# Kernel optimization log

Measured on AMD Instinct MI355X. Metric: run time of the kernel, lower is better.

Reference implementation:

```python
import jax, jax.numpy as jnp
import numpy as np

NUM_STATION = 20
NUM_HEADS = 8
INPUT_DIM = 128
KEY_DIM = 16          # = val_dim = embed_dim // num_heads
EMBED_DIM = 128
NORM = 1.0 / np.sqrt(KEY_DIM).astype(np.float32)


def setup_inputs() -> dict:
    key = jax.random.key(0)
    ks = jax.random.split(key, 10)
    B, N, D = 32, 1024, INPUT_DIM
    q = jax.random.normal(ks[0], (B, N, D), jnp.float32)
    h = jax.random.normal(ks[1], (B, N, D), jnp.float32)
    stdv_k = 1.0 / np.sqrt(KEY_DIM)      # torch init: uniform(-1/sqrt(last_dim), ...)
    stdv_e = 1.0 / np.sqrt(EMBED_DIM)
    def U(k, shape, s):
        return jax.random.uniform(k, shape, jnp.float32, -s, s)
    pshape = (NUM_HEADS, INPUT_DIM, KEY_DIM)
    return {
        "q": q,
        "h": h,
        "W_query_custom": U(ks[2], pshape, stdv_k),
        "W_query_custom_1": U(ks[3], pshape, stdv_k),
        "W_key_custom": U(ks[4], pshape, stdv_k),
        "W_val_custom": U(ks[5], pshape, stdv_k),
        "W_query_charge_1": U(ks[6], pshape, stdv_k),
        "W_key_charge": U(ks[7], pshape, stdv_k),
        "W_val_charge": U(ks[8], pshape, stdv_k),
        "W_out": U(ks[9], (NUM_HEADS, KEY_DIM, EMBED_DIM), stdv_e),
    }


def reference(q, h, W_query_custom, W_query_custom_1, W_key_custom, W_val_custom,
              W_query_charge_1, W_key_charge, W_val_charge, W_out):
    S = NUM_STATION + 1                      # depot + stations
    h_st, h_tk = h[:, :S], h[:, S:]          # [B,S,D], [B,T,D]
    q_st, q_tk = q[:, :S], q[:, S:]

    proj = lambda x, W: jnp.einsum('bnd,hdk->hbnk', x, W)

    K_c = proj(h_tk, W_key_custom)           # [H,B,T,K]
    V_c = proj(h_tk, W_val_custom)
    K_s = proj(h_st, W_key_charge)           # [H,B,S,K]
    V_s = proj(h_st, W_val_charge)

    # task -> task attention (queries via W_query_custom_1)
    Q_tt = proj(q_tk, W_query_custom_1)
    A_tt = jax.nn.softmax(NORM * jnp.einsum('hbqk,hbtk->hbqt', Q_tt, K_c), axis=-1)
    heads_t = jnp.einsum('hbqt,hbtk->hbqk', A_tt, V_c)

    # task -> station attention (queries via W_query_custom)
    Q_ts = proj(q_tk, W_query_custom)
    A_ts = jax.nn.softmax(NORM * jnp.einsum('hbqk,hbsk->hbqs', Q_ts, K_s), axis=-1)
    heads_t = heads_t + jnp.einsum('hbqs,hbsk->hbqk', A_ts, V_s)

    # station -> task attention (queries via W_query_charge_1)
    Q_st = proj(q_st, W_query_charge_1)
    A_st = jax.nn.softmax(NORM * jnp.einsum('hbqk,hbtk->hbqt', Q_st, K_c), axis=-1)
    heads_s = jnp.einsum('hbqt,hbtk->hbqk', A_st, V_c)

    heads = jnp.concatenate([heads_s, heads_t], axis=2)   # [H,B,N,K]
    out = jnp.einsum('hbnk,hke->bne', heads, W_out)        # [B,N,E]
    return out
```

## Files before the change

### kernel.cpp

```cpp
#include <hip/hip_runtime.h>

typedef __bf16 bf16x8 __attribute__((ext_vector_type(8)));
typedef float f32x4 __attribute__((ext_vector_type(4)));
typedef float f32x16 __attribute__((ext_vector_type(16)));
typedef unsigned int uint32;
typedef unsigned short u16;

#define NST 21
#define TOK 1003
#define SCL 0.3606737602222409f

union U4B { uint4 u; bf16x8 b; };

__device__ __forceinline__ uint32 pkbf(float a, float b) {
  uint32 ua = __float_as_uint(a), ub = __float_as_uint(b);
  ua += 0x7fffu + ((ua >> 16) & 1u);
  ub += 0x7fffu + ((ub >> 16) & 1u);
  return (ua >> 16) | (ub & 0xffff0000u);
}
__device__ __forceinline__ u16 bf1(float a) {
  uint32 u = __float_as_uint(a);
  u += 0x7fffu + ((u >> 16) & 1u);
  return (u16)(u >> 16);
}
__device__ __forceinline__ uint32 pkperm(float lo, float hi) {
  return __builtin_amdgcn_perm(__float_as_uint(hi), __float_as_uint(lo), 0x07060302u);
}

__global__ __launch_bounds__(256) void prep(
    const float* __restrict__ q, const float* __restrict__ hx,
    const float* __restrict__ W0, const float* __restrict__ W1,
    const float* __restrict__ W2, const float* __restrict__ W3,
    const float* __restrict__ W4, const float* __restrict__ Wqst,
    const float* __restrict__ Wks, const float* __restrict__ Wvs,
    u16* __restrict__ WtAll, u16* __restrict__ Qm,
    u16* __restrict__ Ks, u16* __restrict__ Vs) {
  int bid = blockIdx.x, tid = threadIdx.x;
  __shared__ float xq2[2][128], xh2[2][128];
  if (bid < 40) {
    int w = bid >> 3, seg = bid & 7;
    const float* W = (w == 0) ? W0 : (w == 1) ? W1 : (w == 2) ? W2
                     : (w == 3) ? W3 : W4;
    u16* dst = WtAll + w * 16384;
#pragma unroll
    for (int it = 0; it < 8; ++it) {
      int i = seg * 2048 + it * 256 + tid;
      int inner = i & 127, outer = i >> 7;
      float v;
      if (w < 4) {
        int h = outer >> 4, k = outer & 15;
        v = W[h * 2048 + inner * 16 + k];
      } else {
        v = W[inner * 128 + outer];
      }
      dst[outer * 128 + inner] = bf1(v);
    }
  } else {
    int t2 = bid - 40;
    int sub = tid >> 7, col = tid & 127;
    int hh = col >> 4, k = col & 15;
    int bs2 = t2 * 2 + sub;
    int b2 = bs2 >> 5, s = bs2 & 31;
    if (s < NST) {
      xq2[sub][col] = q[(size_t)(b2 * 1024 + s) * 128 + col];
      xh2[sub][col] = hx[(size_t)(b2 * 1024 + s) * 128 + col];
    }
    __syncthreads();
    if (s < NST) {
      const float* Wq = Wqst + hh * 2048 + k;
      const float* Wk = Wks + hh * 2048 + k;
      const float* Wv = Wvs + hh * 2048 + k;
      float dq = 0.f, dk_ = 0.f, dv = 0.f;
#pragma unroll 8
      for (int d = 0; d < 128; ++d) {
        float xq = xq2[sub][d], xh = xh2[sub][d];
        dq = fmaf(xq, Wq[d * 16], dq);
        dk_ = fmaf(xh, Wk[d * 16], dk_);
        dv = fmaf(xh, Wv[d * 16], dv);
      }
      Qm[(((size_t)hh * 32 + b2) * 1024 + s) * 16 + k] = bf1(dq * SCL);
      Ks[(((size_t)hh * 32 + b2) * 32 + s) * 16 + k] = bf1(dk_);
      Vs[(((size_t)hh * 32 + b2) * 16 + k) * 32 + s] = bf1(dv);
    } else {
      Ks[(((size_t)hh * 32 + b2) * 32 + s) * 16 + k] = 0;
      Vs[(((size_t)hh * 32 + b2) * 16 + k) * 32 + s] = 0;
    }
  }
}

__global__ __launch_bounds__(256) void proj_pair(
    const float* __restrict__ q, const float* __restrict__ hx,
    const u16* __restrict__ WtAll, u16* __restrict__ Qm,
    u16* __restrict__ Qts, u16* __restrict__ Kc, u16* __restrict__ Vc) {
  __shared__ u16 Wl[128 * 136];
  int pg = blockIdx.x >> 9, mb = blockIdx.x & 511;
  int m0 = mb * 64;
  const float* A = pg ? hx : q;
  int tid = threadIdx.x;
  int wave = tid >> 6, lane = tid & 63;
  int quad = lane >> 4, l15 = lane & 15;
  int mrow = m0 + wave * 16 + l15;

  U4B af[4];
#pragma unroll
  for (int dk = 0; dk < 4; ++dk) {
    const float* Af = A + (size_t)mrow * 128 + dk * 32 + quad * 8;
    float4 a = *(const float4*)Af;
    float4 b = *(const float4*)(Af + 4);
    af[dk].u = make_uint4(pkbf(a.x, a.y), pkbf(a.z, a.w),
                          pkbf(b.x, b.y), pkbf(b.z, b.w));
  }

  int gbase = m0 + wave * 16 + quad * 4;
  int bb = gbase >> 10, n0 = gbase & 1023;

#pragma unroll
  for (int s = 0; s < 2; ++s) {
    int mode = pg * 2 + s;
    const u16* WtG = WtAll + mode * 16384;
    if (s) __syncthreads();
#pragma unroll
    for (int r = 0; r < 8; ++r) {
      int i = r * 256 + tid;
      int e = i >> 4, j = i & 15;
      *(uint4*)&Wl[e * 136 + j * 8] = *(const uint4*)(WtG + e * 128 + j * 8);
    }
    __syncthreads();

    f32x4 c[8];
#pragma unroll
    for (int nt = 0; nt < 8; ++nt)
#pragma unroll
      for (int r = 0; r < 4; ++r) c[nt][r] = 0.f;
#pragma unroll
    for (int dk = 0; dk < 4; ++dk)
#pragma unroll
      for (int nt = 0; nt < 8; ++nt) {
        U4B bg;
        bg.u = *(const uint4*)&Wl[(nt * 16 + l15) * 136 + dk * 32 + quad * 8];
        c[nt] = __builtin_amdgcn_mfma_f32_16x16x32_bf16(af[dk].b, bg.b, c[nt], 0, 0, 0);
      }

    if (mode == 0) {
#pragma unroll
      for (int nt = 0; nt < 8; ++nt)
#pragma unroll
        for (int r = 0; r < 4; ++r) {
          int n = n0 + r;
          if (n < NST) continue;
          Qm[(((size_t)nt * 32 + bb) * 1024 + n) * 16 + l15] = bf1(c[nt][r] * SCL);
        }
    } else if (mode == 1) {
#pragma unroll
      for (int nt = 0; nt < 8; ++nt)
#pragma unroll
        for (int r = 0; r < 4; ++r)
          Qts[(((size_t)nt * 32 + bb) * 1024 + n0 + r) * 16 + l15] =
              bf1(c[nt][r] * SCL);
    } else if (mode == 2) {
#pragma unroll
      for (int nt = 0; nt < 8; ++nt)
#pragma unroll
        for (int r = 0; r < 4; ++r)
          Kc[(((size_t)nt * 32 + bb) * 1024 + n0 + r) * 16 + l15] = bf1(c[nt][r]);
    } else {
#pragma unroll
      for (int nt = 0; nt < 8; ++nt) {
        uint2 w2 = make_uint2(pkbf(c[nt][0], c[nt][1]), pkbf(c[nt][2], c[nt][3]));
        *(uint2*)(Vc + (((size_t)nt * 32 + bb) * 16 + l15) * 1024 + n0) = w2;
      }
    }
  }
}

__global__ __launch_bounds__(256) void outproj(
    const u16* __restrict__ heads, const u16* __restrict__ WtAll,
    float* __restrict__ out) {
  __shared__ u16 Wl[128 * 136];
  const u16* WtG = WtAll + 4 * 16384;
  int tid = threadIdx.x;
#pragma unroll
  for (int r = 0; r < 8; ++r) {
    int i = r * 256 + tid;
    int e = i >> 4, j = i & 15;
    *(uint4*)&Wl[e * 136 + j * 8] = *(const uint4*)(WtG + e * 128 + j * 8);
  }
  __syncthreads();
  int wave = tid >> 6, lane = tid & 63;
  int quad = lane >> 4, l15 = lane & 15;
  int m0 = blockIdx.x * 64;
  int mrow = m0 + wave * 16 + l15;

  f32x4 c[8];
#pragma unroll
  for (int nt = 0; nt < 8; ++nt)
#pragma unroll
    for (int r = 0; r < 4; ++r) c[nt][r] = 0.f;
#pragma unroll
  for (int dk = 0; dk < 4; ++dk) {
    U4B af;
    af.u = *(const uint4*)(heads + (size_t)mrow * 128 + dk * 32 + quad * 8);
#pragma unroll
    for (int nt = 0; nt < 8; ++nt) {
      U4B bg;
      bg.u = *(const uint4*)&Wl[(nt * 16 + l15) * 136 + dk * 32 + quad * 8];
      c[nt] = __builtin_amdgcn_mfma_f32_16x16x32_bf16(af.b, bg.b, c[nt], 0, 0, 0);
    }
  }
  int gbase = m0 + wave * 16 + quad * 4;
#pragma unroll
  for (int nt = 0; nt < 8; ++nt)
#pragma unroll
    for (int r = 0; r < 4; ++r)
      out[(size_t)(gbase + r) * 128 + nt * 16 + l15] = c[nt][r];
}

__global__ __launch_bounds__(256, 8) void attn_main(
    const u16* __restrict__ Qm, const u16* __restrict__ Qts,
    const u16* __restrict__ Kc, const u16* __restrict__ Vc,
    const u16* __restrict__ Ks, const u16* __restrict__ Vs,
    u16* __restrict__ heads) {
  int bx = blockIdx.x;
  int hb = bx & 255, qc = bx >> 8;
  int h = hb >> 5, b = hb & 31;
  int tid = threadIdx.x;
  int wave = tid >> 6, lane = tid & 63;
  int l5 = lane >> 5, l31 = lane & 31;
  int quad = lane >> 4, l15 = lane & 15;

  __shared__ u16 Kl[128 * 26];
  __shared__ u16 Vl[16 * 140];
  __shared__ u16 Pt[4][32 * 36];
  __shared__ u16 KsL[32 * 26];
  __shared__ u16 VsL[16 * 44];

  const u16* Qbase = Qm + ((size_t)(h * 32 + b)) * 16384;
  const u16* QtsB = Qts + ((size_t)(h * 32 + b)) * 16384;
  const u16* Kbase = Kc + ((size_t)(h * 32 + b)) * 16384;
  const u16* Vbase = Vc + ((size_t)(h * 32 + b)) * 16384;
  const u16* KsB = Ks + (size_t)(h * 32 + b) * 512;
  const u16* VsB = Vs + (size_t)(h * 32 + b) * 512;

  if (tid < 64) {
    int key = tid >> 1, half = tid & 1;
    *(uint4*)&KsL[key * 26 + half * 8] = *(const uint4*)(KsB + key * 16 + half * 8);
  } else if (tid < 128) {
    int t = tid - 64;
    int d = t >> 2, kg = t & 3;
    *(uint4*)&VsL[d * 44 + kg * 8] = *(const uint4*)(VsB + d * 32 + kg * 8);
  }

  int qw0 = qc * 128 + wave * 32;
  U4B qf;
  qf.u = *(const uint4*)(Qbase + (size_t)(qw0 + l31) * 16 + l5 * 8);

  int skey = tid >> 1, shalf = tid & 1;
  int sd = tid >> 4, skg = tid & 15;
  uint4 kpre = *(const uint4*)(Kbase + (size_t)skey * 16 + shalf * 8);
  uint4 vpre = *(const uint4*)(Vbase + (size_t)sd * 1024 + skg * 8);

  f32x16 zero16;
#pragma unroll
  for (int i = 0; i < 16; ++i) zero16[i] = 0.f;
  U4B ones;
  ones.u = make_uint4(0x3F803F80u, 0x3F803F80u, 0x3F803F80u, 0x3F803F80u);

  f32x4 o[2], la[2];
#pragma unroll
  for (int mt = 0; mt < 2; ++mt)
#pragma unroll
    for (int r = 0; r < 4; ++r) { o[mt][r] = 0.f; la[mt][r] = 0.f; }

#pragma unroll 1
  for (int kb = 0; kb < 8; ++kb) {
    __syncthreads();
    *(uint4*)&Kl[skey * 26 + shalf * 8] = kpre;
    *(uint4*)&Vl[sd * 140 + skg * 8] = vpre;
    if (kb < 7) {
      int j0n = (kb + 1) * 128;
      kpre = *(const uint4*)(Kbase + (size_t)(j0n + skey) * 16 + shalf * 8);
      vpre = *(const uint4*)(Vbase + (size_t)sd * 1024 + j0n + skg * 8);
    }
    __syncthreads();
#pragma unroll 1
    for (int kt = 0; kt < 4; ++kt) {
      int key0 = kt * 32;
      U4B af;
      af.u = *(const uint4*)&Kl[(key0 + l31) * 26 + l5 * 8];
      f32x16 c0 =
          __builtin_amdgcn_mfma_f32_32x32x16_bf16(af.b, qf.b, zero16, 0, 0, 0);
      bool masked = (kb == 0) && (kt == 0);
#pragma unroll
      for (int g = 0; g < 4; ++g) {
        float p0 = __builtin_amdgcn_exp2f(c0[4 * g + 0]);
        float p1 = __builtin_amdgcn_exp2f(c0[4 * g + 1]);
        float p2 = __builtin_amdgcn_exp2f(c0[4 * g + 2]);
        float p3 = __builtin_amdgcn_exp2f(c0[4 * g + 3]);
        if (masked) {
          int kb0 = 8 * g + 4 * l5;
          p0 = (kb0 + 0 < NST) ? 0.f : p0;
          p1 = (kb0 + 1 < NST) ? 0.f : p1;
          p2 = (kb0 + 2 < NST) ? 0.f : p2;
          p3 = (kb0 + 3 < NST) ? 0.f : p3;
        }
        uint2 w2 = make_uint2(pkperm(p0, p1), pkperm(p2, p3));
        *(uint2*)&Pt[wave][l31 * 36 + 4 * l5 + 8 * g] = w2;
      }
      U4B vf;
      vf.u = *(const uint4*)&Vl[l15 * 140 + key0 + quad * 8];
#pragma unroll
      for (int mt = 0; mt < 2; ++mt) {
        U4B pf;
        pf.u = *(const uint4*)&Pt[wave][(mt * 16 + l15) * 36 + quad * 8];
        o[mt] = __builtin_amdgcn_mfma_f32_16x16x32_bf16(pf.b, vf.b, o[mt], 0, 0, 0);
        la[mt] =
            __builtin_amdgcn_mfma_f32_16x16x32_bf16(pf.b, ones.b, la[mt], 0, 0, 0);
      }
    }
  }

  f32x4 o2[2], la2[2];
#pragma unroll
  for (int mt = 0; mt < 2; ++mt)
#pragma unroll
    for (int r = 0; r < 4; ++r) { o2[mt][r] = 0.f; la2[mt][r] = 0.f; }
  qf.u = *(const uint4*)(QtsB + (size_t)(qw0 + l31) * 16 + l5 * 8);
  {
    U4B af;
    af.u = *(const uint4*)&KsL[l31 * 26 + l5 * 8];
    f32x16 c0 =
        __builtin_amdgcn_mfma_f32_32x32x16_bf16(af.b, qf.b, zero16, 0, 0, 0);
#pragma unroll
    for (int g = 0; g < 4; ++g) {
      float p0 = __builtin_amdgcn_exp2f(c0[4 * g + 0]);
      float p1 = __builtin_amdgcn_exp2f(c0[4 * g + 1]);
      float p2 = __builtin_amdgcn_exp2f(c0[4 * g + 2]);
      float p3 = __builtin_amdgcn_exp2f(c0[4 * g + 3]);
      int kb0 = 8 * g + 4 * l5;
      p0 = (kb0 + 0 >= NST) ? 0.f : p0;
      p1 = (kb0 + 1 >= NST) ? 0.f : p1;
      p2 = (kb0 + 2 >= NST) ? 0.f : p2;
      p3 = (kb0 + 3 >= NST) ? 0.f : p3;
      uint2 w2 = make_uint2(pkperm(p0, p1), pkperm(p2, p3));
      *(uint2*)&Pt[wave][l31 * 36 + 4 * l5 + 8 * g] = w2;
    }
    U4B vf;
    vf.u = *(const uint4*)&VsL[l15 * 44 + quad * 8];
#pragma unroll
    for (int mt = 0; mt < 2; ++mt) {
      U4B pf;
      pf.u = *(const uint4*)&Pt[wave][(mt * 16 + l15) * 36 + quad * 8];
      o2[mt] = __builtin_amdgcn_mfma_f32_16x16x32_bf16(pf.b, vf.b, o2[mt], 0, 0, 0);
      la2[mt] =
          __builtin_amdgcn_mfma_f32_16x16x32_bf16(pf.b, ones.b, la2[mt], 0, 0, 0);
    }
  }

#pragma unroll
  for (int mt = 0; mt < 2; ++mt)
#pragma unroll
    for (int r = 0; r < 4; ++r) {
      int n = qw0 + mt * 16 + quad * 4 + r;
      float val = o[mt][r] * __builtin_amdgcn_rcpf(la[mt][r]);
      if (n >= NST) val += o2[mt][r] * __builtin_amdgcn_rcpf(la2[mt][r]);
      heads[((size_t)b * 1024 + n) * 128 + h * 16 + l15] = bf1(val);
    }
}

extern "C" void kernel_launch(void* const* d_in, const int* in_sizes, int n_in,
                              void* d_out, int out_size, void* d_ws,
                              size_t ws_size, hipStream_t stream) {
  (void)in_sizes; (void)n_in; (void)out_size; (void)ws_size;
  const float* q     = (const float*)d_in[0];
  const float* hx    = (const float*)d_in[1];
  const float* W_qts = (const float*)d_in[2];
  const float* W_qtt = (const float*)d_in[3];
  const float* W_kc  = (const float*)d_in[4];
  const float* W_vc  = (const float*)d_in[5];
  const float* W_qst = (const float*)d_in[6];
  const float* W_ks  = (const float*)d_in[7];
  const float* W_vs  = (const float*)d_in[8];
  const float* W_out = (const float*)d_in[9];

  char* ws = (char*)d_ws;
  u16* heads = (u16*)(ws + 0);
  u16* Qm    = (u16*)(ws + 16777216);
  u16* Qts   = (u16*)(ws + 25165824);
  u16* Kc    = (u16*)(ws + 33554432);
  u16* Vc    = (u16*)(ws + 41943040);
  u16* Ks    = (u16*)(ws + 50331648);
  u16* Vs    = (u16*)(ws + 50593792);
  u16* WtAll = (u16*)(ws + 50855936);

  hipLaunchKernelGGL(prep, dim3(552), dim3(256), 0, stream,
                     q, hx, W_qtt, W_qts, W_kc, W_vc, W_out, W_qst, W_ks, W_vs,
                     WtAll, Qm, Ks, Vs);
  hipLaunchKernelGGL(proj_pair, dim3(1024), dim3(256), 0, stream,
                     q, hx, WtAll, Qm, Qts, Kc, Vc);
  hipLaunchKernelGGL(attn_main, dim3(2048), dim3(256), 0, stream,
                     Qm, Qts, Kc, Vc, Ks, Vs, heads);
  hipLaunchKernelGGL(outproj, dim3(512), dim3(256), 0, stream,
                     heads, WtAll, (float*)d_out);
}
```

Baseline: 169.5 us.

## Keep attention probabilities in registers via permlane32 swap and 32x32 PV MFMA

Removes the per-wave shared-memory staging of the probability tile. The packed bf16 probabilities are rearranged across lanes with v_permlane32_swap and fed straight as the B operand of 32x32x16 MFMAs against V^T. A row of ones is appended to V in LDS so the softmax denominator comes out of the same MFMA, replacing the separate ones-MFMAs. The station-attention pass moves ahead of the main loop, and the output is written with packed vector stores. This cuts LDS traffic and MFMA count but relies on the permlane lane layout being correct and enlarges the V LDS tiles.

```diff
diff --git a/kernel.cpp b/kernel.cpp
--- a/kernel.cpp
+++ b/kernel.cpp
@@ -25,6 +25,15 @@
 }
 __device__ __forceinline__ uint32 pkperm(float lo, float hi) {
   return __builtin_amdgcn_perm(__float_as_uint(hi), __float_as_uint(lo), 0x07060302u);
+}
+__device__ __forceinline__ void plswap(uint32& a, uint32& b) {
+#if __has_builtin(__builtin_amdgcn_permlane32_swap)
+  typedef unsigned int uu2 __attribute__((ext_vector_type(2)));
+  uu2 r = __builtin_amdgcn_permlane32_swap(a, b, false, false);
+  a = r.x; b = r.y;
+#else
+  asm volatile("v_permlane32_swap_b32 %0, %1" : "+v"(a), "+v"(b));
+#endif
 }
 
 __global__ __launch_bounds__(256) void prep(
@@ -226,13 +235,11 @@
   int tid = threadIdx.x;
   int wave = tid >> 6, lane = tid & 63;
   int l5 = lane >> 5, l31 = lane & 31;
-  int quad = lane >> 4, l15 = lane & 15;
 
   __shared__ u16 Kl[128 * 26];
-  __shared__ u16 Vl[16 * 140];
-  __shared__ u16 Pt[4][32 * 36];
+  __shared__ u16 Vl[32 * 140];
   __shared__ u16 KsL[32 * 26];
-  __shared__ u16 VsL[16 * 44];
+  __shared__ u16 VsL[32 * 44];
 
   const u16* Qbase = Qm + ((size_t)(h * 32 + b)) * 16384;
   const u16* QtsB = Qts + ((size_t)(h * 32 + b)) * 16384;
@@ -240,6 +247,8 @@
   const u16* Vbase = Vc + ((size_t)(h * 32 + b)) * 16384;
   const u16* KsB = Ks + (size_t)(h * 32 + b) * 512;
   const u16* VsB = Vs + (size_t)(h * 32 + b) * 512;
+
+  uint4 ones4 = make_uint4(0x3F803F80u, 0x3F803F80u, 0x3F803F80u, 0x3F803F80u);
 
   if (tid < 64) {
     int key = tid >> 1, half = tid & 1;
@@ -248,28 +257,67 @@
     int t = tid - 64;
     int d = t >> 2, kg = t & 3;
     *(uint4*)&VsL[d * 44 + kg * 8] = *(const uint4*)(VsB + d * 32 + kg * 8);
-  }
-
-  int qw0 = qc * 128 + wave * 32;
-  U4B qf;
-  qf.u = *(const uint4*)(Qbase + (size_t)(qw0 + l31) * 16 + l5 * 8);
+  } else if (tid < 192) {
+    int t = tid - 128;
+    *(uint4*)&VsL[(16 + (t >> 2)) * 44 + (t & 3) * 8] = ones4;
+  }
+  *(uint4*)&Vl[(16 + (tid >> 4)) * 140 + (tid & 15) * 8] = ones4;
 
   int skey = tid >> 1, shalf = tid & 1;
   int sd = tid >> 4, skg = tid & 15;
   uint4 kpre = *(const uint4*)(Kbase + (size_t)skey * 16 + shalf * 8);
   uint4 vpre = *(const uint4*)(Vbase + (size_t)sd * 1024 + skg * 8);
 
+  int qw0 = qc * 128 + wave * 32;
+  int qrow = qw0 + l31;
+
   f32x16 zero16;
 #pragma unroll
   for (int i = 0; i < 16; ++i) zero16[i] = 0.f;
-  U4B ones;
-  ones.u = make_uint4(0x3F803F80u, 0x3F803F80u, 0x3F803F80u, 0x3F803F80u);
-
-  f32x4 o[2], la[2];
-#pragma unroll
-  for (int mt = 0; mt < 2; ++mt)
-#pragma unroll
-    for (int r = 0; r < 4; ++r) { o[mt][r] = 0.f; la[mt][r] = 0.f; }
+
+  U4B qf;
+  qf.u = *(const uint4*)(QtsB + (size_t)qrow * 16 + l5 * 8);
+  __syncthreads();
+  float contrib[8];
+  {
+    U4B af;
+    af.u = *(const uint4*)&KsL[l31 * 26 + l5 * 8];
+    f32x16 c0 =
+        __builtin_amdgcn_mfma_f32_32x32x16_bf16(af.b, qf.b, zero16, 0, 0, 0);
+    uint32 w[8];
+#pragma unroll
+    for (int g = 0; g < 4; ++g) {
+      float p0 = __builtin_amdgcn_exp2f(c0[4 * g + 0]);
+      float p1 = __builtin_amdgcn_exp2f(c0[4 * g + 1]);
+      float p2 = __builtin_amdgcn_exp2f(c0[4 * g + 2]);
+      float p3 = __builtin_amdgcn_exp2f(c0[4 * g + 3]);
+      int kb0 = 8 * g + 4 * l5;
+      p0 = (kb0 + 0 >= NST) ? 0.f : p0;
+      p1 = (kb0 + 1 >= NST) ? 0.f : p1;
+      p2 = (kb0 + 2 >= NST) ? 0.f : p2;
+      p3 = (kb0 + 3 >= NST) ? 0.f : p3;
+      w[2 * g] = pkperm(p0, p1);
+      w[2 * g + 1] = pkperm(p2, p3);
+    }
+    plswap(w[0], w[2]); plswap(w[1], w[3]);
+    plswap(w[4], w[6]); plswap(w[5], w[7]);
+    U4B b1, b2, a1, a2;
+    b1.u = make_uint4(w[0], w[1], w[2], w[3]);
+    b2.u = make_uint4(w[4], w[5], w[6], w[7]);
+    a1.u = *(const uint4*)&VsL[l31 * 44 + l5 * 8];
+    a2.u = *(const uint4*)&VsL[l31 * 44 + 16 + l5 * 8];
+    f32x16 acc2 =
+        __builtin_amdgcn_mfma_f32_32x32x16_bf16(a1.b, b1.b, zero16, 0, 0, 0);
+    acc2 = __builtin_amdgcn_mfma_f32_32x32x16_bf16(a2.b, b2.b, acc2, 0, 0, 0);
+    float rla2 = __builtin_amdgcn_rcpf(acc2[8]);
+#pragma unroll
+    for (int r = 0; r < 8; ++r) contrib[r] = acc2[r] * rla2;
+  }
+
+  qf.u = *(const uint4*)(Qbase + (size_t)qrow * 16 + l5 * 8);
+  f32x16 acc;
+#pragma unroll
+  for (int i = 0; i < 16; ++i) acc[i] = 0.f;
 
 #pragma unroll 1
   for (int kb = 0; kb < 8; ++kb) {
@@ -290,6 +338,7 @@
       f32x16 c0 =
           __builtin_amdgcn_mfma_f32_32x32x16_bf16(af.b, qf.b, zero16, 0, 0, 0);
       bool masked = (kb == 0) && (kt == 0);
+      uint32 w[8];
 #pragma unroll
       for (int g = 0; g < 4; ++g) {
         float p0 = __builtin_amdgcn_exp2f(c0[4 * g + 0]);
@@ -303,68 +352,36 @@
           p2 = (kb0 + 2 < NST) ? 0.f : p2;
           p3 = (kb0 + 3 < NST) ? 0.f : p3;
         }
-        uint2 w2 = make_uint2(pkperm(p0, p1), pkperm(p2, p3));
-        *(uint2*)&Pt[wave][l31 * 36 + 4 * l5 + 8 * g] = w2;
+        w[2 * g] = pkperm(p0, p1);
+        w[2 * g + 1] = pkperm(p2, p3);
       }
-      U4B vf;
-      vf.u = *(const uint4*)&Vl[l15 * 140 + key0 + quad * 8];
-#pragma unroll
-      for (int mt = 0; mt < 2; ++mt) {
-        U4B pf;
-        pf.u = *(const uint4*)&Pt[wave][(mt * 16 + l15) * 36 + quad * 8];
-        o[mt] = __builtin_amdgcn_mfma_f32_16x16x32_bf16(pf.b, vf.b, o[mt], 0, 0, 0);
-        la[mt] =
-            __builtin_amdgcn_mfma_f32_16x16x32_bf16(pf.b, ones.b, la[mt], 0, 0, 0);
-      }
-    }
-  }
-
-  f32x4 o2[2], la2[2];
-#pragma unroll
-  for (int mt = 0; mt < 2; ++mt)
-#pragma unroll
-    for (int r = 0; r < 4; ++r) { o2[mt][r] = 0.f; la2[mt][r] = 0.f; }
-  qf.u = *(const uint4*)(QtsB + (size_t)(qw0 + l31) * 16 + l5 * 8);
+      plswap(w[0], w[2]); plswap(w[1], w[3]);
+      plswap(w[4], w[6]); plswap(w[5], w[7]);
+      U4B b1, b2, a1, a2;
+      b1.u = make_uint4(w[0], w[1], w[2], w[3]);
+      b2.u = make_uint4(w[4], w[5], w[6], w[7]);
+      a1.u = *(const uint4*)&Vl[l31 * 140 + key0 + l5 * 8];
+      a2.u = *(const uint4*)&Vl[l31 * 140 + key0 + 16 + l5 * 8];
+      acc = __builtin_amdgcn_mfma_f32_32x32x16_bf16(a1.b, b1.b, acc, 0, 0, 0);
+      acc = __builtin_amdgcn_mfma_f32_32x32x16_bf16(a2.b, b2.b, acc, 0, 0, 0);
+    }
+  }
+
   {
-    U4B af;
-    af.u = *(const uint4*)&KsL[l31 * 26 + l5 * 8];
-    f32x16 c0 =
-        __builtin_amdgcn_mfma_f32_32x32x16_bf16(af.b, qf.b, zero16, 0, 0, 0);
-#pragma unroll
-    for (int g = 0; g < 4; ++g) {
-      float p0 = __builtin_amdgcn_exp2f(c0[4 * g + 0]);
-      float p1 = __builtin_amdgcn_exp2f(c0[4 * g + 1]);
-      float p2 = __builtin_amdgcn_exp2f(c0[4 * g + 2]);
-      float p3 = __builtin_amdgcn_exp2f(c0[4 * g + 3]);
-      int kb0 = 8 * g + 4 * l5;
-      p0 = (kb0 + 0 >= NST) ? 0.f : p0;
-      p1 = (kb0 + 1 >= NST) ? 0.f : p1;
-      p2 = (kb0 + 2 >= NST) ? 0.f : p2;
-      p3 = (kb0 + 3 >= NST) ? 0.f : p3;
-      uint2 w2 = make_uint2(pkperm(p0, p1), pkperm(p2, p3));
-      *(uint2*)&Pt[wave][l31 * 36 + 4 * l5 + 8 * g] = w2;
-    }
-    U4B vf;
-    vf.u = *(const uint4*)&VsL[l15 * 44 + quad * 8];
-#pragma unroll
-    for (int mt = 0; mt < 2; ++mt) {
-      U4B pf;
-      pf.u = *(const uint4*)&Pt[wave][(mt * 16 + l15) * 36 + quad * 8];
-      o2[mt] = __builtin_amdgcn_mfma_f32_16x16x32_bf16(pf.b, vf.b, o2[mt], 0, 0, 0);
-      la2[mt] =
-          __builtin_amdgcn_mfma_f32_16x16x32_bf16(pf.b, ones.b, la2[mt], 0, 0, 0);
-    }
-  }
-
-#pragma unroll
-  for (int mt = 0; mt < 2; ++mt)
-#pragma unroll
-    for (int r = 0; r < 4; ++r) {
-      int n = qw0 + mt * 16 + quad * 4 + r;
-      float val = o[mt][r] * __builtin_amdgcn_rcpf(la[mt][r]);
-      if (n >= NST) val += o2[mt][r] * __builtin_amdgcn_rcpf(la2[mt][r]);
-      heads[((size_t)b * 1024 + n) * 128 + h * 16 + l15] = bf1(val);
-    }
+    float rla = __builtin_amdgcn_rcpf(acc[8]);
+    bool tok = (qrow >= NST);
+    float v0 = acc[0] * rla + (tok ? contrib[0] : 0.f);
+    float v1 = acc[1] * rla + (tok ? contrib[1] : 0.f);
+    float v2 = acc[2] * rla + (tok ? contrib[2] : 0.f);
+    float v3 = acc[3] * rla + (tok ? contrib[3] : 0.f);
+    float v4 = acc[4] * rla + (tok ? contrib[4] : 0.f);
+    float v5 = acc[5] * rla + (tok ? contrib[5] : 0.f);
+    float v6 = acc[6] * rla + (tok ? contrib[6] : 0.f);
+    float v7 = acc[7] * rla + (tok ? contrib[7] : 0.f);
+    u16* hrow = heads + ((size_t)b * 1024 + qrow) * 128 + h * 16;
+    *(uint2*)(hrow + 4 * l5) = make_uint2(pkbf(v0, v1), pkbf(v2, v3));
+    *(uint2*)(hrow + 8 + 4 * l5) = make_uint2(pkbf(v4, v5), pkbf(v6, v7));
+  }
 }
 
 extern "C" void kernel_launch(void* const* d_in, const int* in_sizes, int n_in,
```

After: 160.2 us. 1.06x faster.
